# Performance work log

Measured on AMD Instinct MI355X. Metric: run time of the kernel, lower is better.

Reference implementation:

```python
import jax, jax.numpy as jnp
import numpy as np

B, S, H = 2, 2048, 512
N, D = 8, 64
EPS = 1e-6


def setup_inputs() -> dict:
    key = jax.random.key(0)
    ks = jax.random.split(key, 8)
    scale = 0.02
    return {
        "query": jax.random.normal(ks[0], (B, S, H), jnp.float32),
        "key": jax.random.normal(ks[1], (B, S, H), jnp.float32),
        "value": jax.random.normal(ks[2], (B, S, H), jnp.float32),
        "wq": jax.random.normal(ks[3], (H, N, D), jnp.float32) * scale,
        "bq": jnp.zeros((N, D), jnp.float32),
        "wk": jax.random.normal(ks[4], (H, N, D), jnp.float32) * scale,
        "bk": jnp.zeros((N, D), jnp.float32),
        "wv": jax.random.normal(ks[5], (H, N, D), jnp.float32) * scale,
        "bv": jnp.zeros((N, D), jnp.float32),
        "wo": jax.random.normal(ks[6], (N, D, H), jnp.float32) * scale,
        "bo": jnp.zeros((H,), jnp.float32),
        "step": 0,
    }


def _feature_map(x):
    # elu(x) + 1 (positive feature map for linear attention)
    return jax.nn.elu(x) + 1.0


def reference(query, key, value, wq, bq, wk, bk, wv, bv, wo, bo, step):
    # QKV projections: [B,S,H] -> [B,S,N,D]
    q = jnp.einsum('bsh,hnd->bsnd', query, wq) + bq
    k = jnp.einsum('bsh,hnd->bsnd', key, wk) + bk
    v = jnp.einsum('bsh,hnd->bsnd', value, wv) + bv

    phi_q = _feature_map(q)
    phi_k = _feature_map(k)

    b, s, n, d = k.shape
    # fold batch & heads: [S, B*N, D]
    pq = phi_q.transpose(1, 0, 2, 3).reshape(s, b * n, d)
    pk = phi_k.transpose(1, 0, 2, 3).reshape(s, b * n, d)
    vv = v.transpose(1, 0, 2, 3).reshape(s, b * n, d)

    # causal linear attention via prefix sums
    # state: cumulative sum of outer products phi_k v^T -> [S, B*N, D, D]
    st = jnp.cumsum(jnp.einsum('sbh,sbd->sbhd', pk, vv), axis=0)
    qs = jnp.einsum('sbhd,sbh->sbd', st, pq)
    z = jnp.cumsum(pk, axis=0)
    qz = jnp.einsum('sbh,sbh->sb', pq, z) + EPS
    a_v = qs / qz[..., None]
    a_v = a_v.transpose(1, 0, 2).reshape(b, s, n, d)

    # output projection: [B,S,N,D] -> [B,S,H]
    return jnp.einsum('bsnd,ndh->bsh', a_v, wo) + bo
```

## Files before the change

### kernel.cpp

```cpp
#include <hip/hip_runtime.h>
#include <hip/hip_bf16.h>
#include <cstdint>

#define B_    2
#define S_    2048
#define H_    512
#define N_    8
#define D_    64
#define BS_   4096
#define CHUNK 64
#define NCH   32
#define NBN   16
#define EPS_  1e-6f

typedef __attribute__((ext_vector_type(4))) float  f32x4;
typedef __attribute__((ext_vector_type(8))) short  short8;
typedef __attribute__((ext_vector_type(4))) short  short4_t;

static __device__ __forceinline__ unsigned short f2bf(float x) {
    __hip_bfloat16 h = __float2bfloat16(x);
    return *reinterpret_cast<unsigned short*>(&h);
}
static __device__ __forceinline__ float bf2f(unsigned short u) {
    unsigned int v = ((unsigned int)u) << 16;
    float f;
    __builtin_memcpy(&f, &v, 4);
    return f;
}

__global__ __launch_bounds__(256) void convert_wt_kernel(
    const float* __restrict__ wq, const float* __restrict__ wk,
    const float* __restrict__ wv, const float* __restrict__ wo,
    unsigned short* __restrict__ wqt, unsigned short* __restrict__ wkt,
    unsigned short* __restrict__ wvt, unsigned short* __restrict__ wot)
{
    const int m = blockIdx.z;
    const float* W = (m == 0) ? wq : (m == 1) ? wk : (m == 2) ? wv : wo;
    unsigned short* Wt = (m == 0) ? wqt : (m == 1) ? wkt : (m == 2) ? wvt : wot;

    __shared__ float t[64][65];
    const int k0 = blockIdx.y * 64, c0 = blockIdx.x * 64;
    const int tid = threadIdx.x;
    const int rr = tid >> 6;
    const int cc = tid & 63;
#pragma unroll
    for (int p = 0; p < 16; p++) {
        int kl = rr + p * 4;
        t[kl][cc] = W[(size_t)(k0 + kl) * 512 + c0 + cc];
    }
    __syncthreads();
#pragma unroll
    for (int p = 0; p < 16; p++) {
        int cl = rr + p * 4;
        Wt[(size_t)(c0 + cl) * 512 + k0 + cc] = f2bf(t[cc][cl]);
    }
}

template<int MODE, int BN>
__device__ __forceinline__ void mfma_gemm_body(
    unsigned short (* __restrict__ As)[72], unsigned short (* __restrict__ Bs)[72],
    const void* __restrict__ Xv, const unsigned short* __restrict__ Wt,
    const float* __restrict__ bias,
    unsigned short* __restrict__ Obf, unsigned short* __restrict__ Ot,
    float* __restrict__ Of)
{
    constexpr int NF = BN / 32;
    const int tid  = threadIdx.x;
    const int lane = tid & 63;
    const int w    = tid >> 6;
    const int wm   = (w & 1) * 64;
    const int wn   = (w >> 1) * (BN / 2);
    const int row0 = blockIdx.y * 128;
    const int col0 = blockIdx.x * BN;
    const int frow = lane & 15;
    const int fk   = (lane >> 4) * 8;

    f32x4 acc[4][NF];
#pragma unroll
    for (int m = 0; m < 4; m++)
#pragma unroll
        for (int n = 0; n < NF; n++) acc[m][n] = (f32x4){0.f, 0.f, 0.f, 0.f};

    const int lr = tid >> 3;
    const int lc = (tid & 7) * 8;

    for (int k0 = 0; k0 < 512; k0 += 64) {
#pragma unroll
        for (int p = 0; p < 4; p++) {
            int r = lr + p * 32;
            if (MODE == 3) {
                const unsigned short* X = (const unsigned short*)Xv;
                *reinterpret_cast<short8*>(&As[r][lc]) =
                    *reinterpret_cast<const short8*>(X + (size_t)(row0 + r) * 512 + k0 + lc);
            } else {
                const float* X = (const float*)Xv;
                const float* src = X + (size_t)(row0 + r) * 512 + k0 + lc;
                float4 x0 = *reinterpret_cast<const float4*>(src);
                float4 x1 = *reinterpret_cast<const float4*>(src + 4);
                short8 o;
                o[0] = (short)f2bf(x0.x); o[1] = (short)f2bf(x0.y);
                o[2] = (short)f2bf(x0.z); o[3] = (short)f2bf(x0.w);
                o[4] = (short)f2bf(x1.x); o[5] = (short)f2bf(x1.y);
                o[6] = (short)f2bf(x1.z); o[7] = (short)f2bf(x1.w);
                *reinterpret_cast<short8*>(&As[r][lc]) = o;
            }
        }
#pragma unroll
        for (int p = 0; p < BN / 32; p++) {
            int r = (tid >> 3) + p * 32;
            *reinterpret_cast<short8*>(&Bs[r][lc]) =
                *reinterpret_cast<const short8*>(Wt + (size_t)(col0 + r) * 512 + k0 + lc);
        }
        __syncthreads();
#pragma unroll
        for (int kk = 0; kk < 64; kk += 32) {
            short8 a[4], b[NF];
#pragma unroll
            for (int m = 0; m < 4; m++)
                a[m] = *reinterpret_cast<const short8*>(&As[wm + m * 16 + frow][kk + fk]);
#pragma unroll
            for (int n = 0; n < NF; n++)
                b[n] = *reinterpret_cast<const short8*>(&Bs[wn + n * 16 + frow][kk + fk]);
#pragma unroll
            for (int m = 0; m < 4; m++)
#pragma unroll
                for (int n = 0; n < NF; n++)
                    acc[m][n] = __builtin_amdgcn_mfma_f32_16x16x32_bf16(
                        a[m], b[n], acc[m][n], 0, 0, 0);
        }
        __syncthreads();
    }

#pragma unroll
    for (int n = 0; n < NF; n++) {
        int col = col0 + wn + n * 16 + frow;
        float bv_ = bias[col];
#pragma unroll
        for (int m = 0; m < 4; m++) {
            int rbase = row0 + wm + m * 16 + (lane >> 4) * 4;
            short4_t t4;
#pragma unroll
            for (int r = 0; r < 4; r++) {
                float val = acc[m][n][r] + bv_;
                if (MODE == 0 || MODE == 1)
                    val = (val > 0.f) ? (val + 1.f) : __expf(val);
                if (MODE == 3) {
                    Of[(size_t)(rbase + r) * 512 + col] = val;
                } else {
                    unsigned short ub = f2bf(val);
                    t4[r] = (short)ub;
                    if (MODE == 0 || MODE == 1)
                        Obf[(size_t)(rbase + r) * 512 + col] = ub;
                }
            }
            if (MODE == 1 || MODE == 2) {
                int bb = rbase >> 11;
                int t_ = rbase & 2047;
                *reinterpret_cast<short4_t*>(
                    Ot + (size_t)bb * (512 * 2048) + (size_t)col * 2048 + t_) = t4;
            }
        }
    }
}

__global__ __launch_bounds__(256) void qkv_proj_kernel(
    const float* __restrict__ q_in, const float* __restrict__ k_in,
    const float* __restrict__ v_in,
    const unsigned short* __restrict__ wqt, const unsigned short* __restrict__ wkt,
    const unsigned short* __restrict__ wvt,
    const float* __restrict__ bq, const float* __restrict__ bk, const float* __restrict__ bv,
    unsigned short* __restrict__ pq, unsigned short* __restrict__ pk,
    unsigned short* __restrict__ pkT, unsigned short* __restrict__ pvT)
{
    __shared__ unsigned short As[128][72];
    __shared__ unsigned short Bs[128][72];
    int m = blockIdx.z;
    if (m == 0)      mfma_gemm_body<0, 128>(As, Bs, q_in, wqt, bq, pq, nullptr, nullptr);
    else if (m == 1) mfma_gemm_body<1, 128>(As, Bs, k_in, wkt, bk, pk, pkT, nullptr);
    else             mfma_gemm_body<2, 128>(As, Bs, v_in, wvt, bv, nullptr, pvT, nullptr);
}

__global__ __launch_bounds__(256) void out_proj_kernel(
    const unsigned short* __restrict__ avb, const unsigned short* __restrict__ wot,
    const float* __restrict__ bo, float* __restrict__ out)
{
    __shared__ unsigned short As[128][72];
    __shared__ unsigned short Bs[64][72];
    mfma_gemm_body<3, 64>(As, Bs, avb, wot, bo, nullptr, nullptr, out);
}

__global__ __launch_bounds__(256) void chunk_kvscan_kernel(
    const unsigned short* __restrict__ pkT, const unsigned short* __restrict__ pvT,
    unsigned short* __restrict__ Mb, float* __restrict__ zb)
{
    __shared__ float waveTot[4][256];
    __shared__ float zTot[4][16];

    const int tile = blockIdx.x;
    const int bn   = blockIdx.y;
    const int d0   = (tile >> 2) * 16;
    const int h0   = (tile & 3) * 16;
    const int b = bn >> 3, n = bn & 7;
    const int tid = threadIdx.x, lane = tid & 63, w = tid >> 6;
    const int frow = lane & 15, grp = lane >> 4, fk = grp * 8;
    const bool do_z = (tile >> 2) == 0;

    const size_t vrow = (size_t)b * (512 * 2048) + (size_t)(n * 64 + d0 + frow) * 2048;
    const size_t krow = (size_t)b * (512 * 2048) + (size_t)(n * 64 + h0 + frow) * 2048;

    f32x4 run = (f32x4){0.f, 0.f, 0.f, 0.f};
    f32x4 loc[8];
    float runz = 0.f, locz[8];

#pragma unroll
    for (int c = 0; c < 8; c++) {
        int t0 = (w * 8 + c) * 64;
        loc[c] = run;
        locz[c] = runz;
        short8 a0 = *reinterpret_cast<const short8*>(pvT + vrow + t0 + fk);
        short8 a1 = *reinterpret_cast<const short8*>(pvT + vrow + t0 + 32 + fk);
        short8 b0 = *reinterpret_cast<const short8*>(pkT + krow + t0 + fk);
        short8 b1 = *reinterpret_cast<const short8*>(pkT + krow + t0 + 32 + fk);
        run = __builtin_amdgcn_mfma_f32_16x16x32_bf16(a0, b0, run, 0, 0, 0);
        run = __builtin_amdgcn_mfma_f32_16x16x32_bf16(a1, b1, run, 0, 0, 0);
        if (do_z) {
            float zp = 0.f;
#pragma unroll
            for (int j = 0; j < 8; j++) zp += bf2f((unsigned short)b0[j]) + bf2f((unsigned short)b1[j]);
            zp += __shfl_xor(zp, 16);
            zp += __shfl_xor(zp, 32);
            runz += zp;
        }
    }

#pragma unroll
    for (int r = 0; r < 4; r++)
        waveTot[w][(grp * 4 + r) * 16 + frow] = run[r];
    if (do_z && lane < 16) zTot[w][frow] = runz;
    __syncthreads();

    f32x4 carry = (f32x4){0.f, 0.f, 0.f, 0.f};
    float carryz = 0.f;
    for (int pw = 0; pw < w; pw++) {
#pragma unroll
        for (int r = 0; r < 4; r++)
            carry[r] += waveTot[pw][(grp * 4 + r) * 16 + frow];
        carryz += zTot[pw][frow];
    }

#pragma unroll
    for (int c = 0; c < 8; c++) {
        size_t mbase = ((size_t)bn * NCH + (w * 8 + c)) * 4096;
#pragma unroll
        for (int r = 0; r < 4; r++)
            Mb[mbase + (size_t)(d0 + grp * 4 + r) * 64 + h0 + frow] = f2bf(carry[r] + loc[c][r]);
        if (do_z && lane < 16)
            zb[((size_t)bn * NCH + (w * 8 + c)) * 64 + h0 + frow] = carryz + locz[c];
    }
}

__global__ __launch_bounds__(256) void chunk_attn_kernel(
    const unsigned short* __restrict__ pq, const unsigned short* __restrict__ pk,
    const unsigned short* __restrict__ pvT, const unsigned short* __restrict__ Mb,
    const float* __restrict__ zb, unsigned short* __restrict__ av)
{
    __shared__ unsigned short Qs[64][72], Ks[64][72], VT[64][72], Ab[64][72];
    __shared__ float zs[64], dqz4[64][4], dAS[64];

    const int c = blockIdx.x, bn = blockIdx.y;
    const int b = bn >> 3, n = bn & 7;
    const int row0 = b * S_ + c * 64;
    const int col0 = n * 64;
    const int t0 = c * 64;
    const size_t vbase = (size_t)b * 512 * 2048;
    const size_t mbase = ((size_t)bn * NCH + c) * 4096;
    const int tid = threadIdx.x, lane = tid & 63, w = tid >> 6;

#pragma unroll
    for (int p = 0; p < 2; p++) {
        int r  = (tid >> 3) + p * 32;
        int c8 = (tid & 7) * 8;
        *reinterpret_cast<short8*>(&Qs[r][c8]) =
            *reinterpret_cast<const short8*>(pq + (size_t)(row0 + r) * 512 + col0 + c8);
        *reinterpret_cast<short8*>(&Ks[r][c8]) =
            *reinterpret_cast<const short8*>(pk + (size_t)(row0 + r) * 512 + col0 + c8);
        *reinterpret_cast<short8*>(&VT[r][c8]) =
            *reinterpret_cast<const short8*>(pvT + vbase + (size_t)(col0 + r) * 2048 + t0 + c8);
    }
    if (tid < 64) zs[tid] = zb[((size_t)bn * NCH + c) * 64 + tid];
    __syncthreads();

    const int frow = lane & 15, grp = lane >> 4, fk = grp * 8;
    const int srow = w * 16;

    f32x4 a1[4];
#pragma unroll
    for (int tf = 0; tf < 4; tf++) a1[tf] = (f32x4){0.f, 0.f, 0.f, 0.f};
#pragma unroll
    for (int ks = 0; ks < 2; ks++) {
        short8 qa = *reinterpret_cast<const short8*>(&Qs[srow + frow][ks * 32 + fk]);
#pragma unroll
        for (int tf = 0; tf < 4; tf++) {
            short8 kb = *reinterpret_cast<const short8*>(&Ks[tf * 16 + frow][ks * 32 + fk]);
            a1[tf] = __builtin_amdgcn_mfma_f32_16x16x32_bf16(qa, kb, a1[tf], 0, 0, 0);
        }
    }

    float rs[4] = {0.f, 0.f, 0.f, 0.f};
#pragma unroll
    for (int tf = 0; tf < 4; tf++) {
        int t_ = tf * 16 + frow;
#pragma unroll
        for (int r = 0; r < 4; r++) {
            int s_ = srow + grp * 4 + r;
            float v = (t_ <= s_) ? a1[tf][r] : 0.f;
            rs[r] += v;
            Ab[s_][t_] = f2bf(v);
        }
    }
#pragma unroll
    for (int msk = 1; msk < 16; msk <<= 1)
#pragma unroll
        for (int r = 0; r < 4; r++) rs[r] += __shfl_xor(rs[r], msk);
    if (frow == 0) {
#pragma unroll
        for (int r = 0; r < 4; r++) dAS[srow + grp * 4 + r] = rs[r];
    }

    {
        int s = tid & 63, part = tid >> 6;
        float sdq = 0.f;
#pragma unroll
        for (int j = 0; j < 16; j++) {
            int h = part * 16 + j;
            sdq += bf2f(Qs[s][h]) * zs[h];
        }
        dqz4[s][part] = sdq;
    }
    __syncthreads();

    f32x4 o[4];
#pragma unroll
    for (int df = 0; df < 4; df++) o[df] = (f32x4){0.f, 0.f, 0.f, 0.f};
#pragma unroll
    for (int ks = 0; ks < 2; ks++) {
        short8 aa = *reinterpret_cast<const short8*>(&Ab[srow + frow][ks * 32 + fk]);
        short8 qa = *reinterpret_cast<const short8*>(&Qs[srow + frow][ks * 32 + fk]);
#pragma unroll
        for (int df = 0; df < 4; df++) {
            short8 vb = *reinterpret_cast<const short8*>(&VT[df * 16 + frow][ks * 32 + fk]);
            short8 sp = *reinterpret_cast<const short8*>(
                Mb + mbase + (size_t)(df * 16 + frow) * 64 + ks * 32 + fk);
            o[df] = __builtin_amdgcn_mfma_f32_16x16x32_bf16(aa, vb, o[df], 0, 0, 0);
            o[df] = __builtin_amdgcn_mfma_f32_16x16x32_bf16(qa, sp, o[df], 0, 0, 0);
        }
    }

    float inv[4];
    size_t obase[4];
#pragma unroll
    for (int r = 0; r < 4; r++) {
        int s_loc = srow + grp * 4 + r;
        float dq = dqz4[s_loc][0] + dqz4[s_loc][1] + dqz4[s_loc][2] + dqz4[s_loc][3];
        inv[r] = 1.f / (dq + dAS[s_loc] + EPS_);
        int s_b = c * 64 + s_loc;
        int jj  = n * S_ + s_b;
        obase[r] = (size_t)(b * S_ + (jj >> 3)) * 512 + (size_t)(jj & 7) * 64;
    }
#pragma unroll
    for (int df = 0; df < 4; df++) {
        int d = df * 16 + frow;
#pragma unroll
        for (int r = 0; r < 4; r++)
            av[obase[r] + d] = f2bf(o[df][r] * inv[r]);
    }
}

extern "C" void kernel_launch(void* const* d_in, const int* in_sizes, int n_in,
                              void* d_out, int out_size, void* d_ws, size_t ws_size,
                              hipStream_t stream)
{
    const float* q_in = (const float*)d_in[0];
    const float* k_in = (const float*)d_in[1];
    const float* v_in = (const float*)d_in[2];
    const float* wq   = (const float*)d_in[3];
    const float* bq   = (const float*)d_in[4];
    const float* wk   = (const float*)d_in[5];
    const float* bk   = (const float*)d_in[6];
    const float* wv   = (const float*)d_in[7];
    const float* bv   = (const float*)d_in[8];
    const float* wo   = (const float*)d_in[9];
    const float* bo   = (const float*)d_in[10];
    float* out = (float*)d_out;

    const size_t PLANE = (size_t)BS_ * 512;

    float* ws = (float*)d_ws;
    float* zbuf = ws;
    unsigned short* u16 = (unsigned short*)(zbuf + 32768);
    unsigned short* Mb  = u16;
    unsigned short* pq  = Mb  + PLANE;
    unsigned short* pk  = pq  + PLANE;
    unsigned short* pkT = pk  + PLANE;
    unsigned short* pvT = pkT + PLANE;
    unsigned short* avb = pvT + PLANE;
    unsigned short* wqt = avb + PLANE;
    unsigned short* wkt = wqt + 262144;
    unsigned short* wvt = wkt + 262144;
    unsigned short* wot = wvt + 262144;

    convert_wt_kernel<<<dim3(8, 8, 4), 256, 0, stream>>>(wq, wk, wv, wo, wqt, wkt, wvt, wot);
    qkv_proj_kernel<<<dim3(4, 32, 3), 256, 0, stream>>>(
        q_in, k_in, v_in, wqt, wkt, wvt, bq, bk, bv, pq, pk, pkT, pvT);
    chunk_kvscan_kernel<<<dim3(16, NBN), 256, 0, stream>>>(pkT, pvT, Mb, zbuf);
    chunk_attn_kernel<<<dim3(NCH, NBN), 256, 0, stream>>>(pq, pk, pvT, Mb, zbuf, avb);
    out_proj_kernel<<<dim3(8, 32), 256, 0, stream>>>(avb, wot, bo, out);
}
```

Measured before the change: 145.3 us.

## Fuse output projection into chunked attention kernel via shared-memory staging

Drops the separate out_proj kernel and the bf16 attention-output buffer. Each chunk-attention block writes its 64x64 normalized attention tile into shared memory, laid out as 8 output rows of 512 features, which works because of the reference's odd reshape. It then multiplies that tile by the output weights with MFMA and writes fp32 results plus bias directly. This saves one launch and a round trip to global memory, but each block reads its wot slice straight from global memory, and half of each M=16 MFMA tile is wasted since only 8 rows are valid.

Result: slower. 165.8 us (+14.1%).

```diff
diff --git a/kernel.cpp b/kernel.cpp
--- a/kernel.cpp
+++ b/kernel.cpp
@@ -56,30 +56,28 @@
     }
 }
 
-template<int MODE, int BN>
+template<int MODE>
 __device__ __forceinline__ void mfma_gemm_body(
     unsigned short (* __restrict__ As)[72], unsigned short (* __restrict__ Bs)[72],
     const void* __restrict__ Xv, const unsigned short* __restrict__ Wt,
     const float* __restrict__ bias,
-    unsigned short* __restrict__ Obf, unsigned short* __restrict__ Ot,
-    float* __restrict__ Of)
-{
-    constexpr int NF = BN / 32;
+    unsigned short* __restrict__ Obf, unsigned short* __restrict__ Ot)
+{
     const int tid  = threadIdx.x;
     const int lane = tid & 63;
     const int w    = tid >> 6;
     const int wm   = (w & 1) * 64;
-    const int wn   = (w >> 1) * (BN / 2);
+    const int wn   = (w >> 1) * 64;
     const int row0 = blockIdx.y * 128;
-    const int col0 = blockIdx.x * BN;
+    const int col0 = blockIdx.x * 128;
     const int frow = lane & 15;
     const int fk   = (lane >> 4) * 8;
 
-    f32x4 acc[4][NF];
+    f32x4 acc[4][4];
 #pragma unroll
     for (int m = 0; m < 4; m++)
 #pragma unroll
-        for (int n = 0; n < NF; n++) acc[m][n] = (f32x4){0.f, 0.f, 0.f, 0.f};
+        for (int n = 0; n < 4; n++) acc[m][n] = (f32x4){0.f, 0.f, 0.f, 0.f};
 
     const int lr = tid >> 3;
     const int lc = (tid & 7) * 8;
@@ -88,25 +86,19 @@
 #pragma unroll
         for (int p = 0; p < 4; p++) {
             int r = lr + p * 32;
-            if (MODE == 3) {
-                const unsigned short* X = (const unsigned short*)Xv;
-                *reinterpret_cast<short8*>(&As[r][lc]) =
-                    *reinterpret_cast<const short8*>(X + (size_t)(row0 + r) * 512 + k0 + lc);
-            } else {
-                const float* X = (const float*)Xv;
-                const float* src = X + (size_t)(row0 + r) * 512 + k0 + lc;
-                float4 x0 = *reinterpret_cast<const float4*>(src);
-                float4 x1 = *reinterpret_cast<const float4*>(src + 4);
-                short8 o;
-                o[0] = (short)f2bf(x0.x); o[1] = (short)f2bf(x0.y);
-                o[2] = (short)f2bf(x0.z); o[3] = (short)f2bf(x0.w);
-                o[4] = (short)f2bf(x1.x); o[5] = (short)f2bf(x1.y);
-                o[6] = (short)f2bf(x1.z); o[7] = (short)f2bf(x1.w);
-                *reinterpret_cast<short8*>(&As[r][lc]) = o;
-            }
-        }
-#pragma unroll
-        for (int p = 0; p < BN / 32; p++) {
+            const float* X = (const float*)Xv;
+            const float* src = X + (size_t)(row0 + r) * 512 + k0 + lc;
+            float4 x0 = *reinterpret_cast<const float4*>(src);
+            float4 x1 = *reinterpret_cast<const float4*>(src + 4);
+            short8 o;
+            o[0] = (short)f2bf(x0.x); o[1] = (short)f2bf(x0.y);
+            o[2] = (short)f2bf(x0.z); o[3] = (short)f2bf(x0.w);
+            o[4] = (short)f2bf(x1.x); o[5] = (short)f2bf(x1.y);
+            o[6] = (short)f2bf(x1.z); o[7] = (short)f2bf(x1.w);
+            *reinterpret_cast<short8*>(&As[r][lc]) = o;
+        }
+#pragma unroll
+        for (int p = 0; p < 4; p++) {
             int r = (tid >> 3) + p * 32;
             *reinterpret_cast<short8*>(&Bs[r][lc]) =
                 *reinterpret_cast<const short8*>(Wt + (size_t)(col0 + r) * 512 + k0 + lc);
@@ -114,17 +106,17 @@
         __syncthreads();
 #pragma unroll
         for (int kk = 0; kk < 64; kk += 32) {
-            short8 a[4], b[NF];
+            short8 a[4], b[4];
 #pragma unroll
             for (int m = 0; m < 4; m++)
                 a[m] = *reinterpret_cast<const short8*>(&As[wm + m * 16 + frow][kk + fk]);
 #pragma unroll
-            for (int n = 0; n < NF; n++)
+            for (int n = 0; n < 4; n++)
                 b[n] = *reinterpret_cast<const short8*>(&Bs[wn + n * 16 + frow][kk + fk]);
 #pragma unroll
             for (int m = 0; m < 4; m++)
 #pragma unroll
-                for (int n = 0; n < NF; n++)
+                for (int n = 0; n < 4; n++)
                     acc[m][n] = __builtin_amdgcn_mfma_f32_16x16x32_bf16(
                         a[m], b[n], acc[m][n], 0, 0, 0);
         }
@@ -132,7 +124,7 @@
     }
 
 #pragma unroll
-    for (int n = 0; n < NF; n++) {
+    for (int n = 0; n < 4; n++) {
         int col = col0 + wn + n * 16 + frow;
         float bv_ = bias[col];
 #pragma unroll
@@ -144,14 +136,10 @@
                 float val = acc[m][n][r] + bv_;
                 if (MODE == 0 || MODE == 1)
                     val = (val > 0.f) ? (val + 1.f) : __expf(val);
-                if (MODE == 3) {
-                    Of[(size_t)(rbase + r) * 512 + col] = val;
-                } else {
-                    unsigned short ub = f2bf(val);
-                    t4[r] = (short)ub;
-                    if (MODE == 0 || MODE == 1)
-                        Obf[(size_t)(rbase + r) * 512 + col] = ub;
-                }
+                unsigned short ub = f2bf(val);
+                t4[r] = (short)ub;
+                if (MODE == 0 || MODE == 1)
+                    Obf[(size_t)(rbase + r) * 512 + col] = ub;
             }
             if (MODE == 1 || MODE == 2) {
                 int bb = rbase >> 11;
@@ -175,18 +163,9 @@
     __shared__ unsigned short As[128][72];
     __shared__ unsigned short Bs[128][72];
     int m = blockIdx.z;
-    if (m == 0)      mfma_gemm_body<0, 128>(As, Bs, q_in, wqt, bq, pq, nullptr, nullptr);
-    else if (m == 1) mfma_gemm_body<1, 128>(As, Bs, k_in, wkt, bk, pk, pkT, nullptr);
-    else             mfma_gemm_body<2, 128>(As, Bs, v_in, wvt, bv, nullptr, pvT, nullptr);
-}
-
-__global__ __launch_bounds__(256) void out_proj_kernel(
-    const unsigned short* __restrict__ avb, const unsigned short* __restrict__ wot,
-    const float* __restrict__ bo, float* __restrict__ out)
-{
-    __shared__ unsigned short As[128][72];
-    __shared__ unsigned short Bs[64][72];
-    mfma_gemm_body<3, 64>(As, Bs, avb, wot, bo, nullptr, nullptr, out);
+    if (m == 0)      mfma_gemm_body<0>(As, Bs, q_in, wqt, bq, pq, nullptr);
+    else if (m == 1) mfma_gemm_body<1>(As, Bs, k_in, wkt, bk, pk, pkT);
+    else             mfma_gemm_body<2>(As, Bs, v_in, wvt, bv, nullptr, pvT);
 }
 
 __global__ __launch_bounds__(256) void chunk_kvscan_kernel(
@@ -259,13 +238,19 @@
     }
 }
 
-__global__ __launch_bounds__(256) void chunk_attn_kernel(
+__global__ __launch_bounds__(256) void chunk_attn_out_kernel(
     const unsigned short* __restrict__ pq, const unsigned short* __restrict__ pk,
     const unsigned short* __restrict__ pvT, const unsigned short* __restrict__ Mb,
-    const float* __restrict__ zb, unsigned short* __restrict__ av)
-{
-    __shared__ unsigned short Qs[64][72], Ks[64][72], VT[64][72], Ab[64][72];
+    const float* __restrict__ zb, const unsigned short* __restrict__ wot,
+    const float* __restrict__ bo, float* __restrict__ out)
+{
+    __shared__ unsigned short Qs[64][72], Ks[64][72];
+    __shared__ unsigned short UN[9216];
     __shared__ float zs[64], dqz4[64][4], dAS[64];
+
+    unsigned short (* __restrict__ VT)[72]  = (unsigned short(*)[72])UN;
+    unsigned short (* __restrict__ Ab)[72]  = (unsigned short(*)[72])(UN + 4608);
+    unsigned short (* __restrict__ av8)[520] = (unsigned short(*)[520])UN;
 
     const int c = blockIdx.x, bn = blockIdx.y;
     const int b = bn >> 3, n = bn & 7;
@@ -357,22 +342,51 @@
     }
 
     float inv[4];
-    size_t obase[4];
 #pragma unroll
     for (int r = 0; r < 4; r++) {
         int s_loc = srow + grp * 4 + r;
         float dq = dqz4[s_loc][0] + dqz4[s_loc][1] + dqz4[s_loc][2] + dqz4[s_loc][3];
         inv[r] = 1.f / (dq + dAS[s_loc] + EPS_);
-        int s_b = c * 64 + s_loc;
-        int jj  = n * S_ + s_b;
-        obase[r] = (size_t)(b * S_ + (jj >> 3)) * 512 + (size_t)(jj & 7) * 64;
-    }
+    }
+
+    __syncthreads();
+
 #pragma unroll
     for (int df = 0; df < 4; df++) {
         int d = df * 16 + frow;
 #pragma unroll
-        for (int r = 0; r < 4; r++)
-            av[obase[r] + d] = f2bf(o[df][r] * inv[r]);
+        for (int r = 0; r < 4; r++) {
+            int s_loc = srow + grp * 4 + r;
+            av8[s_loc >> 3][(s_loc & 7) * 64 + d] = f2bf(o[df][r] * inv[r]);
+        }
+    }
+    __syncthreads();
+
+    f32x4 oacc[8];
+#pragma unroll
+    for (int nf = 0; nf < 8; nf++) oacc[nf] = (f32x4){0.f, 0.f, 0.f, 0.f};
+    for (int ks2 = 0; ks2 < 16; ks2++) {
+        int j0 = ks2 * 32;
+        short8 a = *reinterpret_cast<const short8*>(&av8[frow][j0 + fk]);
+#pragma unroll
+        for (int nf = 0; nf < 8; nf++) {
+            int h = w * 128 + nf * 16 + frow;
+            short8 bfr = *reinterpret_cast<const short8*>(wot + (size_t)h * 512 + j0 + fk);
+            oacc[nf] = __builtin_amdgcn_mfma_f32_16x16x32_bf16(a, bfr, oacc[nf], 0, 0, 0);
+        }
+    }
+    const int orow0 = b * S_ + n * 256 + c * 8;
+    if (grp < 2) {
+#pragma unroll
+        for (int nf = 0; nf < 8; nf++) {
+            int h = w * 128 + nf * 16 + frow;
+            float bb_ = bo[h];
+#pragma unroll
+            for (int r = 0; r < 4; r++) {
+                int row = grp * 4 + r;
+                out[(size_t)(orow0 + row) * 512 + h] = oacc[nf][r] + bb_;
+            }
+        }
     }
 }
 
@@ -403,8 +417,7 @@
     unsigned short* pk  = pq  + PLANE;
     unsigned short* pkT = pk  + PLANE;
     unsigned short* pvT = pkT + PLANE;
-    unsigned short* avb = pvT + PLANE;
-    unsigned short* wqt = avb + PLANE;
+    unsigned short* wqt = pvT + PLANE;
     unsigned short* wkt = wqt + 262144;
     unsigned short* wvt = wkt + 262144;
     unsigned short* wot = wvt + 262144;
@@ -413,6 +426,6 @@
     qkv_proj_kernel<<<dim3(4, 32, 3), 256, 0, stream>>>(
         q_in, k_in, v_in, wqt, wkt, wvt, bq, bk, bv, pq, pk, pkT, pvT);
     chunk_kvscan_kernel<<<dim3(16, NBN), 256, 0, stream>>>(pkT, pvT, Mb, zbuf);
-    chunk_attn_kernel<<<dim3(NCH, NBN), 256, 0, stream>>>(pq, pk, pvT, Mb, zbuf, avb);
-    out_proj_kernel<<<dim3(8, 32), 256, 0, stream>>>(avb, wot, bo, out);
-}
+    chunk_attn_out_kernel<<<dim3(NCH, NBN), 256, 0, stream>>>(
+        pq, pk, pvT, Mb, zbuf, wot, bo, out);
+}
```
